# Kernel optimization log

Hardware: AMD Instinct MI355X
Metric: run time of the kernel (lower is better)

Reference implementation:

```python
import jax, jax.numpy as jnp
import numpy as np
import math

B, S, D, H, DK, DFF = 64, 512, 512, 8, 64, 2048


def _layernorm(x, g, b, eps=1e-5):
    mu = jnp.mean(x, axis=-1, keepdims=True)
    var = jnp.var(x, axis=-1, keepdims=True)
    return (x - mu) * jax.lax.rsqrt(var + eps) * g + b


def setup_inputs() -> dict:
    key = jax.random.key(0)
    ks = jax.random.split(key, 16)
    std = 0.02
    return {
        "query": jax.random.normal(ks[0], (B, S, D), jnp.float32),
        "key": jax.random.normal(ks[1], (B, S, D), jnp.float32),
        "values": jax.random.normal(ks[2], (B, S, D), jnp.float32),
        "forget_rate": jax.random.uniform(ks[3], (B, 1, S, 1), jnp.float32),
        "Wq": jax.random.normal(ks[4], (D, D), jnp.float32) * std,
        "bq": jnp.zeros((D,), jnp.float32),
        "Wk": jax.random.normal(ks[5], (D, D), jnp.float32) * std,
        "bk": jnp.zeros((D,), jnp.float32),
        "Wv": jax.random.normal(ks[6], (D, D), jnp.float32) * std,
        "bv": jnp.zeros((D,), jnp.float32),
        "Wo": jax.random.normal(ks[7], (D, D), jnp.float32) * std,
        "bo": jnp.zeros((D,), jnp.float32),
        "g1": jnp.ones((D,), jnp.float32),
        "beta1": jnp.zeros((D,), jnp.float32),
        "W1": jax.random.normal(ks[8], (D, DFF), jnp.float32) * std,
        "bf1": jnp.zeros((DFF,), jnp.float32),
        "W2": jax.random.normal(ks[9], (DFF, D), jnp.float32) * std,
        "bf2": jnp.zeros((D,), jnp.float32),
        "g2": jnp.ones((D,), jnp.float32),
        "beta2": jnp.zeros((D,), jnp.float32),
        "mask": 0,
    }


def reference(query, key, values, forget_rate, Wq, bq, Wk, bk, Wv, bv, Wo, bo,
              g1, beta1, W1, bf1, W2, bf2, g2, beta2, mask):
    bs, seqlen, _ = query.shape
    # project and split heads -> [B, H, S, DK]
    q = (query @ Wq + bq).reshape(bs, seqlen, H, DK).transpose(0, 2, 1, 3)
    k = (key @ Wk + bk).reshape(bs, seqlen, H, DK).transpose(0, 2, 1, 3)
    v = (values @ Wv + bv).reshape(bs, seqlen, H, DK).transpose(0, 2, 1, 3)

    scores = jnp.einsum('bhqd,bhkd->bhqk', q, k) / math.sqrt(DK)  # [B,H,S,S]
    # forget_rate [B,1,S,1] broadcasts over heads and key dim (== repeat in torch)
    scores = scores * forget_rate
    # src_mask: allowed where triu(ones, k=mask) == 0, i.e. j < i + mask
    allowed = jnp.tril(jnp.ones((seqlen, seqlen), bool), mask - 1)
    scores = jnp.where(allowed, scores, jnp.float32(-1e32))
    probs = jax.nn.softmax(scores, axis=-1)
    if mask == 0:  # zero_pad: overwrite first query row with zeros
        probs = probs.at[:, :, 0, :].set(0.0)
    out = jnp.einsum('bhqk,bhkd->bhqd', probs, v)  # [B,H,S,DK]
    concat = out.transpose(0, 2, 1, 3).reshape(bs, seqlen, D)
    attn_out = concat @ Wo + bo

    x = _layernorm(query + attn_out, g1, beta1)
    ff = jax.nn.relu(x @ W1 + bf1) @ W2 + bf2
    x = _layernorm(x + ff, g2, beta2)
    return x
```

## Files before the change

### kernel.cpp

```cpp
#include <hip/hip_runtime.h>
#include <hip/hip_bf16.h>
#include <stdint.h>

typedef __attribute__((ext_vector_type(8))) short short8;
typedef __attribute__((ext_vector_type(8))) unsigned short ushort8;
typedef __attribute__((ext_vector_type(4))) unsigned short ushort4v;
typedef __attribute__((ext_vector_type(4))) float f32x4;

#define DEV static __device__ __forceinline__

constexpr int Bc = 64, Sc = 512, Dc = 512, Hc = 8, DKc = 64, DFc = 2048;
constexpr int Mtot = Bc * Sc;
constexpr int CB   = 16;
constexpr int RC   = CB * Sc;

DEV unsigned short f2b(float f) {
    union { float f; unsigned u; } x; x.f = f;
    unsigned r = x.u + 0x7fffu + ((x.u >> 16) & 1u);
    return (unsigned short)(r >> 16);
}
DEV float b2f(unsigned short u) {
    union { unsigned u; float f; } x; x.u = ((unsigned)u) << 16; return x.f;
}

DEV void gload16(const void* g, void* l) {
    __builtin_amdgcn_global_load_lds(
        (const __attribute__((address_space(1))) void*)g,
        (__attribute__((address_space(3))) void*)l, 16, 0, 0);
}

__global__ void k_cvt(const float* __restrict__ in, unsigned short* __restrict__ out, int n8) {
    int idx = blockIdx.x * 256 + threadIdx.x;
    if (idx >= n8) return;
    const float4* p = (const float4*)(in + (size_t)idx * 8);
    float4 a = p[0], b = p[1];
    ushort8 o;
    o[0] = f2b(a.x); o[1] = f2b(a.y); o[2] = f2b(a.z); o[3] = f2b(a.w);
    o[4] = f2b(b.x); o[5] = f2b(b.y); o[6] = f2b(b.z); o[7] = f2b(b.w);
    *(ushort8*)(out + (size_t)idx * 8) = o;
}

__global__ void k_copy8(const unsigned short* __restrict__ in, unsigned short* __restrict__ out, int n8) {
    int idx = blockIdx.x * 256 + threadIdx.x;
    if (idx >= n8) return;
    *(ushort8*)(out + (size_t)idx * 8) = *(const ushort8*)(in + (size_t)idx * 8);
}

__global__ void k_cvt_w_all(
    const float* __restrict__ Wq, const float* __restrict__ Wk, const float* __restrict__ Wv,
    const float* __restrict__ Wo, const float* __restrict__ W1, const float* __restrict__ W2,
    unsigned short* __restrict__ Wqt, unsigned short* __restrict__ Wkt,
    unsigned short* __restrict__ Wvt, unsigned short* __restrict__ Wot,
    unsigned short* __restrict__ W1t, unsigned short* __restrict__ W2t) {
    int idx = blockIdx.x * 256 + threadIdx.x;
    const float* in; unsigned short* out; int K, N, li;
    if (idx < 131072) {
        int w = idx >> 15, r = idx & 32767;
        const float* ins[4] = {Wq, Wk, Wv, Wo};
        unsigned short* outs[4] = {Wqt, Wkt, Wvt, Wot};
        in = ins[w]; out = outs[w]; K = 512; N = 512; li = r;
    } else if (idx < 262144) {
        in = W1; out = W1t; K = 512; N = 2048; li = idx - 131072;
    } else {
        in = W2; out = W2t; K = 2048; N = 512; li = idx - 262144;
    }
    int kc = li % (K / 8), n = li / (K / 8);
    ushort8 o;
    #pragma unroll
    for (int j = 0; j < 8; ++j) o[j] = f2b(in[(size_t)(kc * 8 + j) * N + n]);
    *(ushort8*)(out + (size_t)n * K + kc * 8) = o;
}

__global__ void k_cvt_all(
    const float* __restrict__ Wq, const float* __restrict__ Wk, const float* __restrict__ Wv,
    const float* __restrict__ Wo, const float* __restrict__ W1, const float* __restrict__ W2,
    unsigned short* __restrict__ Wqt, unsigned short* __restrict__ Wkt,
    unsigned short* __restrict__ Wvt, unsigned short* __restrict__ Wot,
    unsigned short* __restrict__ W1t, unsigned short* __restrict__ W2t,
    const float* __restrict__ q_in, const float* __restrict__ k_in, const float* __restrict__ v_in,
    unsigned short* __restrict__ q_out, unsigned short* __restrict__ k_out,
    unsigned short* __restrict__ v_out) {
    int idx = blockIdx.x * 256 + threadIdx.x;
    if (idx >= 393216) {
        int a = idx - 393216;
        const float* in; unsigned short* out; int li;
        if (a < 2097152)       { in = q_in; out = q_out; li = a; }
        else if (a < 4194304)  { in = k_in; out = k_out; li = a - 2097152; }
        else                   { in = v_in; out = v_out; li = a - 4194304; }
        const float4* p = (const float4*)(in + (size_t)li * 8);
        float4 x = p[0], y = p[1];
        ushort8 o;
        o[0] = f2b(x.x); o[1] = f2b(x.y); o[2] = f2b(x.z); o[3] = f2b(x.w);
        o[4] = f2b(y.x); o[5] = f2b(y.y); o[6] = f2b(y.z); o[7] = f2b(y.w);
        *(ushort8*)(out + (size_t)li * 8) = o;
        return;
    }
    const float* in; unsigned short* out; int K, N, li;
    if (idx < 131072) {
        int w = idx >> 15, r = idx & 32767;
        const float* ins[4] = {Wq, Wk, Wv, Wo};
        unsigned short* outs[4] = {Wqt, Wkt, Wvt, Wot};
        in = ins[w]; out = outs[w]; K = 512; N = 512; li = r;
    } else if (idx < 262144) {
        in = W1; out = W1t; K = 512; N = 2048; li = idx - 131072;
    } else {
        in = W2; out = W2t; K = 2048; N = 512; li = idx - 262144;
    }
    int kc = li % (K / 8), n = li / (K / 8);
    ushort8 o;
    #pragma unroll
    for (int j = 0; j < 8; ++j) o[j] = f2b(in[(size_t)(kc * 8 + j) * N + n]);
    *(ushort8*)(out + (size_t)n * K + kc * 8) = o;
}

template<int BM, int BN>
DEV void gemm_core(const unsigned short* __restrict__ A, int lda,
                   const unsigned short* __restrict__ Bt, int ldb, int K,
                   unsigned short* lA, unsigned short* lB,
                   f32x4 (&acc)[BM / 32][BN / 32]) {
    constexpr int MF = BM / 32, NF = BN / 32;
    const int tid = threadIdx.x, lane = tid & 63, wv = tid >> 6;
    const int wr = wv >> 1, wc = wv & 1;
    const int l15 = lane & 15, l4 = lane >> 4, l7 = l15 & 7;
    #pragma unroll
    for (int mf = 0; mf < MF; ++mf)
        #pragma unroll
        for (int nf = 0; nf < NF; ++nf)
            acc[mf][nf] = f32x4{0.f, 0.f, 0.f, 0.f};

    auto stage = [&](int buf, int kt0) {
        unsigned short* dA = lA + (size_t)buf * BM * 64;
        #pragma unroll
        for (int r = 0; r < BM / 32; ++r) {
            int c = r * 256 + tid, row = c >> 3, gs = c & 7;
            gload16(A + (size_t)row * lda + kt0 + ((gs ^ (row & 7)) * 8),
                    dA + (size_t)(r * 256 + wv * 64) * 8);
        }
        unsigned short* dB = lB + (size_t)buf * BN * 64;
        #pragma unroll
        for (int r = 0; r < BN / 32; ++r) {
            int c = r * 256 + tid, row = c >> 3, gs = c & 7;
            gload16(Bt + (size_t)row * ldb + kt0 + ((gs ^ (row & 7)) * 8),
                    dB + (size_t)(r * 256 + wv * 64) * 8);
        }
    };

    stage(0, 0);
    __syncthreads();
    const int nk = K / 64;
    for (int t = 0; t < nk; ++t) {
        const int buf = t & 1;
        if (t + 1 < nk) stage(buf ^ 1, (t + 1) * 64);
        const unsigned short* cA = lA + (size_t)buf * BM * 64;
        const unsigned short* cB = lB + (size_t)buf * BN * 64;
        #pragma unroll
        for (int kt = 0; kt < 2; ++kt) {
            short8 af[MF], bfr[NF];
            #pragma unroll
            for (int mf = 0; mf < MF; ++mf)
                af[mf] = *(const short8*)&cA[(wr * (BM / 2) + mf * 16 + l15) * 64 +
                                             (((kt * 4 + l4) ^ l7) * 8)];
            #pragma unroll
            for (int nf = 0; nf < NF; ++nf)
                bfr[nf] = *(const short8*)&cB[(wc * (BN / 2) + nf * 16 + l15) * 64 +
                                              (((kt * 4 + l4) ^ l7) * 8)];
            #pragma unroll
            for (int mf = 0; mf < MF; ++mf)
                #pragma unroll
                for (int nf = 0; nf < NF; ++nf)
                    acc[mf][nf] = __builtin_amdgcn_mfma_f32_16x16x32_bf16(af[mf], bfr[nf], acc[mf][nf], 0, 0, 0);
        }
        __syncthreads();
    }
}

__global__ __launch_bounds__(256) void k_gemm_qkv(
    const unsigned short* __restrict__ X, const unsigned short* __restrict__ Wt,
    const float* __restrict__ bias, unsigned short* __restrict__ out, int which) {
    __shared__ unsigned short lA[2 * 128 * 64], lB[2 * 128 * 64];
    int m0 = blockIdx.x * 128, n0 = blockIdx.y * 128;
    f32x4 acc[4][4];
    gemm_core<128, 128>(X + (size_t)m0 * Dc, Dc, Wt + (size_t)n0 * Dc, Dc, Dc, lA, lB, acc);
    const int lane = threadIdx.x & 63, wv = threadIdx.x >> 6;
    const int wr = wv >> 1, wc = wv & 1, l15 = lane & 15, l4 = lane >> 4;
    #pragma unroll
    for (int mf = 0; mf < 4; ++mf) {
        #pragma unroll
        for (int nf = 0; nf < 4; ++nf) {
            int n = n0 + wc * 64 + nf * 16 + l15;
            int h = n >> 6, dk = n & 63;
            float bv = bias[n];
            if (which == 2) {
                int mg = m0 + wr * 64 + mf * 16 + l4 * 4;
                int b = mg >> 9, s = mg & 511;
                ushort4v o;
                #pragma unroll
                for (int r = 0; r < 4; ++r) o[r] = f2b(acc[mf][nf][r] + bv);
                *(ushort4v*)&out[((size_t)(b * Hc + h) * DKc + dk) * Sc + s] = o;
            } else {
                float scale = (which == 0) ? 0.125f : 1.0f;
                #pragma unroll
                for (int r = 0; r < 4; ++r) {
                    int mg = m0 + wr * 64 + mf * 16 + l4 * 4 + r;
                    int b = mg >> 9, s = mg & 511;
                    out[((size_t)(b * Hc + h) * Sc + s) * DKc + dk] = f2b((acc[mf][nf][r] + bv) * scale);
                }
            }
        }
    }
}

__global__ __launch_bounds__(256) void k_flash(
    const unsigned short* __restrict__ Qb, const unsigned short* __restrict__ Kb,
    const unsigned short* __restrict__ Vt, unsigned short* __restrict__ conc,
    const float* __restrict__ fr, const int* __restrict__ maskp, int b_base) {
    __shared__ unsigned short lKb[2][64 * 64];
    __shared__ unsigned short lVb[2][64 * 64];
    __shared__ unsigned short lP[128 * 64];
    const int head = blockIdx.y, bl = head >> 3, h = head & 7;
    const int bg = b_base + bl;
    const int m0 = blockIdx.x * 128;
    const int mv = *maskp;
    const int tid = threadIdx.x, lane = tid & 63, w = tid >> 6;
    const int l15 = lane & 15, l4 = lane >> 4;
    const int l7 = l15 & 7;
    const int rw = w * 32;
    constexpr float LOG2E = 1.44269504088896340736f;

    unsigned short* lQ = &lKb[0][0];
    const unsigned short* Qg = Qb + ((size_t)head * Sc + m0) * DKc;
    #pragma unroll
    for (int r = 0; r < 4; ++r) {
        int c = r * 256 + tid, row = c >> 3, gs = c & 7;
        gload16(Qg + (size_t)row * DKc + ((gs ^ (row & 7)) * 8), lQ + (size_t)(r * 256 + w * 64) * 8);
    }
    __syncthreads();
    short8 qf[2][2];
    #pragma unroll
    for (int kt = 0; kt < 2; ++kt)
        #pragma unroll
        for (int mf = 0; mf < 2; ++mf)
            qf[kt][mf] = *(const short8*)&lQ[(rw + mf * 16 + l15) * 64 + (((kt * 4 + l4) ^ l7) * 8)];
    float frr[8];
    #pragma unroll
    for (int mf = 0; mf < 2; ++mf)
        #pragma unroll
        for (int r = 0; r < 4; ++r)
            frr[mf * 4 + r] = fr[(size_t)bg * Sc + m0 + rw + mf * 16 + l4 * 4 + r] * LOG2E;
    __syncthreads();

    f32x4 accO[2][4];
    #pragma unroll
    for (int mf = 0; mf < 2; ++mf)
        #pragma unroll
        for (int nf = 0; nf < 4; ++nf)
            accO[mf][nf] = f32x4{0.f, 0.f, 0.f, 0.f};
    float l_run[8];
    #pragma unroll
    for (int i = 0; i < 8; ++i) l_run[i] = 0.f;

    const unsigned short* Kg0 = Kb + (size_t)head * Sc * DKc;
    const unsigned short* Vg0 = Vt + (size_t)head * DKc * Sc;
    int nt = ((m0 + 126 + mv) >> 7) + 1;
    if (nt > 4) nt = 4;
    if (nt < 1) nt = 1;
    const int nc = nt * 2;

    {
        const unsigned short* Kg = Kg0;
        const unsigned short* Vg = Vg0;
        #pragma unroll
        for (int r = 0; r < 2; ++r) {
            int c = r * 256 + tid, row = c >> 3, gs = c & 7;
            gload16(Kg + (size_t)row * DKc + ((gs ^ (row & 7)) * 8), &lKb[0][0] + (size_t)(r * 256 + w * 64) * 8);
            gload16(Vg + (size_t)row * Sc + ((gs ^ (row & 7)) * 8), &lVb[0][0] + (size_t)(r * 256 + w * 64) * 8);
        }
    }
    __syncthreads();

    for (int ci = 0; ci < nc; ++ci) {
        const int buf = ci & 1;
        if (ci + 1 < nc) {
            int n1 = (ci + 1) * 64;
            const unsigned short* Kg = Kg0 + (size_t)n1 * DKc;
            const unsigned short* Vg = Vg0 + n1;
            #pragma unroll
            for (int r = 0; r < 2; ++r) {
                int c = r * 256 + tid, row = c >> 3, gs = c & 7;
                gload16(Kg + (size_t)row * DKc + ((gs ^ (row & 7)) * 8),
                        &lKb[buf ^ 1][0] + (size_t)(r * 256 + w * 64) * 8);
                gload16(Vg + (size_t)row * Sc + ((gs ^ (row & 7)) * 8),
                        &lVb[buf ^ 1][0] + (size_t)(r * 256 + w * 64) * 8);
            }
        }
        const int n0c = ci * 64;
        short8 bk[4][2];
        #pragma unroll
        for (int j = 0; j < 4; ++j)
            #pragma unroll
            for (int kt = 0; kt < 2; ++kt)
                bk[j][kt] = *(const short8*)&lKb[buf][(j * 16 + l15) * 64 + (((kt * 4 + l4) ^ l7) * 8)];
        #pragma unroll
        for (int mf = 0; mf < 2; ++mf) {
            f32x4 sa[4];
            #pragma unroll
            for (int j = 0; j < 4; ++j) sa[j] = f32x4{0.f, 0.f, 0.f, 0.f};
            #pragma unroll
            for (int kt = 0; kt < 2; ++kt)
                #pragma unroll
                for (int j = 0; j < 4; ++j)
                    sa[j] = __builtin_amdgcn_mfma_f32_16x16x32_bf16(qf[kt][mf], bk[j][kt], sa[j], 0, 0, 0);
            #pragma unroll
            for (int r = 0; r < 4; ++r) {
                int rowl = rw + mf * 16 + l4 * 4 + r;
                int rowg = m0 + rowl;
                int prs = rowl & 7;
                float fres = frr[mf * 4 + r];
                float ps = 0.f;
                #pragma unroll
                for (int j = 0; j < 4; ++j) {
                    int colg = n0c + j * 16 + l15;
                    float p = (colg < rowg + mv) ? exp2f(sa[j][r] * fres) : 0.f;
                    ps += p;
                    int gw = j * 2 + (l15 >> 3);
                    lP[rowl * 64 + ((gw ^ prs) * 8) + l7] = f2b(p);
                }
                l_run[mf * 4 + r] += ps;
            }
        }
        #pragma unroll
        for (int kl = 0; kl < 2; ++kl) {
            short8 pa[2];
            #pragma unroll
            for (int mf = 0; mf < 2; ++mf)
                pa[mf] = *(const short8*)&lP[(rw + mf * 16 + l15) * 64 + (((kl * 4 + l4) ^ l7) * 8)];
            #pragma unroll
            for (int nf = 0; nf < 4; ++nf) {
                short8 bv8 = *(const short8*)&lVb[buf][(nf * 16 + l15) * 64 + (((kl * 4 + l4) ^ l7) * 8)];
                #pragma unroll
                for (int mf = 0; mf < 2; ++mf)
                    accO[mf][nf] = __builtin_amdgcn_mfma_f32_16x16x32_bf16(pa[mf], bv8, accO[mf][nf], 0, 0, 0);
            }
        }
        __syncthreads();
    }
    #pragma unroll
    for (int mf = 0; mf < 2; ++mf)
        #pragma unroll
        for (int r = 0; r < 4; ++r) {
            int rowg = m0 + rw + mf * 16 + l4 * 4 + r;
            float l = l_run[mf * 4 + r];
            #pragma unroll
            for (int o = 1; o < 16; o <<= 1) l += __shfl_xor(l, o);
            float inv = (rowg + mv > 0) ? 1.0f / l : 0.f;
            #pragma unroll
            for (int nf = 0; nf < 4; ++nf) {
                int dk = nf * 16 + l15;
                conc[((size_t)bg * Sc + rowg) * Dc + h * DKc + dk] = f2b(accO[mf][nf][r] * inv);
            }
        }
}

__global__ __launch_bounds__(256) void k_wo(
    const unsigned short* __restrict__ Cc, const unsigned short* __restrict__ Wot,
    const float* __restrict__ bo, const float* __restrict__ query, float* __restrict__ y) {
    __shared__ unsigned short lA[2 * 128 * 64], lB[2 * 128 * 64];
    int m0 = blockIdx.x * 128, n0 = blockIdx.y * 128;
    f32x4 acc[4][4];
    gemm_core<128, 128>(Cc + (size_t)m0 * Dc, Dc, Wot + (size_t)n0 * Dc, Dc, Dc, lA, lB, acc);
    const int lane = threadIdx.x & 63, wv = threadIdx.x >> 6;
    const int wr = wv >> 1, wc = wv & 1, l15 = lane & 15, l4 = lane >> 4;
    #pragma unroll
    for (int mf = 0; mf < 4; ++mf)
        #pragma unroll
        for (int nf = 0; nf < 4; ++nf) {
            int n = n0 + wc * 64 + nf * 16 + l15;
            float bv = bo[n];
            #pragma unroll
            for (int r = 0; r < 4; ++r) {
                int m = m0 + wr * 64 + mf * 16 + l4 * 4 + r;
                y[(size_t)m * Dc + n] = acc[mf][nf][r] + bv + query[(size_t)m * Dc + n];
            }
        }
}

__global__ __launch_bounds__(256) void k_ff1(
    const unsigned short* __restrict__ X, const unsigned short* __restrict__ W1t,
    const float* __restrict__ b1, unsigned short* __restrict__ hb) {
    __shared__ unsigned short lA[2 * 128 * 64], lB[2 * 128 * 64];
    int m0 = blockIdx.x * 128, n0 = blockIdx.y * 128;
    f32x4 acc[4][4];
    gemm_core<128, 128>(X + (size_t)m0 * Dc, Dc, W1t + (size_t)n0 * Dc, Dc, Dc, lA, lB, acc);
    const int lane = threadIdx.x & 63, wv = threadIdx.x >> 6;
    const int wr = wv >> 1, wc = wv & 1, l15 = lane & 15, l4 = lane >> 4;
    #pragma unroll
    for (int mf = 0; mf < 4; ++mf)
        #pragma unroll
        for (int nf = 0; nf < 4; ++nf) {
            int n = n0 + wc * 64 + nf * 16 + l15;
            float bv = b1[n];
            #pragma unroll
            for (int r = 0; r < 4; ++r) {
                int m = m0 + wr * 64 + mf * 16 + l4 * 4 + r;
                hb[(size_t)m * DFc + n] = f2b(fmaxf(acc[mf][nf][r] + bv, 0.f));
            }
        }
}

__global__ __launch_bounds__(256) void k_ff2b(
    const unsigned short* __restrict__ Hb, const unsigned short* __restrict__ W2t,
    const float* __restrict__ b2, const unsigned short* __restrict__ residb,
    float* __restrict__ y) {
    __shared__ unsigned short lA[2 * 128 * 64], lB[2 * 128 * 64];
    int m0 = blockIdx.x * 128, n0 = blockIdx.y * 128;
    f32x4 acc[4][4];
    gemm_core<128, 128>(Hb + (size_t)m0 * DFc, DFc, W2t + (size_t)n0 * DFc, DFc, DFc, lA, lB, acc);
    const int lane = threadIdx.x & 63, wv = threadIdx.x >> 6;
    const int wr = wv >> 1, wc = wv & 1, l15 = lane & 15, l4 = lane >> 4;
    #pragma unroll
    for (int mf = 0; mf < 4; ++mf)
        #pragma unroll
        for (int nf = 0; nf < 4; ++nf) {
            int n = n0 + wc * 64 + nf * 16 + l15;
            float bv = b2[n];
            #pragma unroll
            for (int r = 0; r < 4; ++r) {
                int m = m0 + wr * 64 + mf * 16 + l4 * 4 + r;
                y[(size_t)m * Dc + n] = acc[mf][nf][r] + bv + b2f(residb[(size_t)m * Dc + n]);
            }
        }
}

__global__ __launch_bounds__(256) void k_ln(
    const float* __restrict__ in, const float* __restrict__ g, const float* __restrict__ be,
    float* __restrict__ outf, unsigned short* __restrict__ outb) {
    int rid = blockIdx.x * 4 + (threadIdx.x >> 6);
    int lane = threadIdx.x & 63;
    const float* row = in + (size_t)rid * Dc;
    float4 a = ((const float4*)row)[lane * 2];
    float4 b = ((const float4*)row)[lane * 2 + 1];
    float x[8] = {a.x, a.y, a.z, a.w, b.x, b.y, b.z, b.w};
    float s = 0.f, ss = 0.f;
    #pragma unroll
    for (int j = 0; j < 8; ++j) { s += x[j]; ss += x[j] * x[j]; }
    #pragma unroll
    for (int o = 1; o < 64; o <<= 1) { s += __shfl_xor(s, o); ss += __shfl_xor(ss, o); }
    float mu = s * (1.f / 512.f);
    float var = ss * (1.f / 512.f) - mu * mu;
    float rs = rsqrtf(var + 1e-5f);
    float4 g0 = ((const float4*)g)[lane * 2], g1v = ((const float4*)g)[lane * 2 + 1];
    float4 e0 = ((const float4*)be)[lane * 2], e1 = ((const float4*)be)[lane * 2 + 1];
    float gg[8] = {g0.x, g0.y, g0.z, g0.w, g1v.x, g1v.y, g1v.z, g1v.w};
    float ee[8] = {e0.x, e0.y, e0.z, e0.w, e1.x, e1.y, e1.z, e1.w};
    float o8[8];
    #pragma unroll
    for (int j = 0; j < 8; ++j) o8[j] = (x[j] - mu) * rs * gg[j] + ee[j];
    if (outf) {
        float4* po = (float4*)(outf + (size_t)rid * Dc);
        float4 w0 = {o8[0], o8[1], o8[2], o8[3]}, w1 = {o8[4], o8[5], o8[6], o8[7]};
        po[lane * 2] = w0; po[lane * 2 + 1] = w1;
    }
    if (outb) {
        ushort8 ob;
        #pragma unroll
        for (int j = 0; j < 8; ++j) ob[j] = f2b(o8[j]);
        *(ushort8*)(outb + (size_t)rid * Dc + lane * 8) = ob;
    }
}

extern "C" void kernel_launch(void* const* d_in, const int* in_sizes, int n_in,
                              void* d_out, int out_size, void* d_ws, size_t ws_size,
                              hipStream_t stream) {
    const float* query = (const float*)d_in[0];
    const float* key_  = (const float*)d_in[1];
    const float* vals  = (const float*)d_in[2];
    const float* fr    = (const float*)d_in[3];
    const float* Wq = (const float*)d_in[4];  const float* bq = (const float*)d_in[5];
    const float* Wk = (const float*)d_in[6];  const float* bk = (const float*)d_in[7];
    const float* Wv = (const float*)d_in[8];  const float* bv = (const float*)d_in[9];
    const float* Wo = (const float*)d_in[10]; const float* bo = (const float*)d_in[11];
    const float* g1 = (const float*)d_in[12]; const float* be1 = (const float*)d_in[13];
    const float* W1 = (const float*)d_in[14]; const float* b1 = (const float*)d_in[15];
    const float* W2 = (const float*)d_in[16]; const float* b2 = (const float*)d_in[17];
    const float* g2 = (const float*)d_in[18]; const float* be2 = (const float*)d_in[19];
    const int* maskp = (const int*)d_in[20];
    float* out = (float*)d_out;

    char* ab = (char*)d_out;
    unsigned short* xb    = (unsigned short*)ab;
    unsigned short* conc  = (unsigned short*)ab;
    unsigned short* x1b   = conc;
    unsigned short* keyst = (unsigned short*)(ab + (size_t)32 * 1048576);
    unsigned short* Qc   = (unsigned short*)(ab + (size_t)32 * 1048576);
    unsigned short* Kc   = (unsigned short*)(ab + (size_t)40 * 1048576);
    unsigned short* Vc   = (unsigned short*)(ab + (size_t)48 * 1048576);
    unsigned short* xst  = (unsigned short*)(ab + (size_t)56 * 1048576);
    float*          xfc  = (float*)(ab + (size_t)32 * 1048576);

    char* ws = (char*)d_ws;
    unsigned short* Wqt = (unsigned short*)ws;
    unsigned short* Wkt = Wqt + 512 * 512;
    unsigned short* Wvt = Wkt + 512 * 512;
    unsigned short* Wot = Wvt + 512 * 512;
    unsigned short* W1t = Wot + 512 * 512;
    unsigned short* W2t = W1t + 2048 * 512;
    char* wend = (char*)(W2t + 512 * 2048);
    size_t wrem = (ws_size > (size_t)(wend - ws)) ? ws_size - (size_t)(wend - ws) : 0;
    const size_t qkvb = (size_t)Mtot * Dc * 2;

    const bool bigpath = (wrem >= 3 * qkvb);

    const float* acts[3] = {query, key_, vals};
    const unsigned short* wt3[3] = {Wqt, Wkt, Wvt};
    const float* bs3[3] = {bq, bk, bv};

    if (bigpath) {
        unsigned short* QbF = (unsigned short*)wend;
        unsigned short* KbF = QbF + qkvb / 2;
        unsigned short* VtF = KbF + qkvb / 2;
        unsigned short* hb     = QbF;
        unsigned short* resid0 = VtF;
        float*          xf     = (float*)KbF;
        const int Mc = 16384;

        k_cvt_all<<<dim3(26112), dim3(256), 0, stream>>>(
            Wq, Wk, Wv, Wo, W1, W2, Wqt, Wkt, Wvt, Wot, W1t, W2t,
            query, key_, vals, xb, keyst, KbF);

        k_gemm_qkv<<<dim3(Mtot / 128, 4), dim3(256), 0, stream>>>(KbF,   Wvt, bv, VtF, 2);
        k_gemm_qkv<<<dim3(Mtot / 128, 4), dim3(256), 0, stream>>>(keyst, Wkt, bk, KbF, 1);
        k_gemm_qkv<<<dim3(Mtot / 128, 4), dim3(256), 0, stream>>>(xb,    Wqt, bq, QbF, 0);

        k_flash<<<dim3(Sc / 128, Bc * Hc), dim3(256), 0, stream>>>(QbF, KbF, VtF, conc, fr, maskp, 0);

        k_wo<<<dim3(Mtot / 128, 4), dim3(256), 0, stream>>>(conc, Wot, bo, query, xf);
        k_ln<<<dim3(Mtot / 4), dim3(256), 0, stream>>>(xf, g1, be1, (float*)nullptr, x1b);

        k_copy8<<<dim3(Mc / 4), dim3(256), 0, stream>>>(x1b, resid0, Mc * Dc / 8);

        for (int mb = Mtot - Mc; mb >= 0; mb -= Mc) {
            k_ff1<<<dim3(Mc / 128, 16), dim3(256), 0, stream>>>(x1b + (size_t)mb * Dc, W1t, b1, hb);
            k_ff2b<<<dim3(Mc / 128, 4), dim3(256), 0, stream>>>(hb, W2t, b2,
                                                                mb ? x1b + (size_t)mb * Dc : resid0,
                                                                out + (size_t)mb * Dc);
            k_ln<<<dim3(Mc / 4), dim3(256), 0, stream>>>(out + (size_t)mb * Dc, g2, be2,
                                                         out + (size_t)mb * Dc, (unsigned short*)nullptr);
        }
    } else {
        int Mc = 128;
        for (int c = 8192; c >= 128; c >>= 1)
            if ((size_t)c * 5120 <= wrem) { Mc = c; break; }
        unsigned short* hb     = (unsigned short*)wend;
        unsigned short* resid0 = (unsigned short*)(wend + (size_t)Mc * 4096);

        k_cvt_w_all<<<dim3(1536), dim3(256), 0, stream>>>(Wq, Wk, Wv, Wo, W1, W2,
                                                          Wqt, Wkt, Wvt, Wot, W1t, W2t);
        unsigned short* out3[3] = {Qc, Kc, Vc};
        for (int cb = 0; cb < Bc / CB; ++cb) {
            for (int p = 0; p < 3; ++p) {
                k_cvt<<<dim3(RC * Dc / 8 / 256), dim3(256), 0, stream>>>(
                    acts[p] + (size_t)cb * RC * Dc, xst, RC * Dc / 8);
                k_gemm_qkv<<<dim3(RC / 128, 4), dim3(256), 0, stream>>>(xst, wt3[p], bs3[p], out3[p], p);
            }
            k_flash<<<dim3(Sc / 128, CB * Hc), dim3(256), 0, stream>>>(Qc, Kc, Vc, conc, fr, maskp, cb * CB);
        }
        for (int hp = 0; hp < 2; ++hp) {
            int mb = hp * 16384;
            k_wo<<<dim3(16384 / 128, 4), dim3(256), 0, stream>>>(conc + (size_t)mb * Dc, Wot, bo,
                                                                 query + (size_t)mb * Dc, xfc);
            k_ln<<<dim3(16384 / 4), dim3(256), 0, stream>>>(xfc, g1, be1, (float*)nullptr,
                                                            x1b + (size_t)mb * Dc);
        }
        k_copy8<<<dim3(Mc / 4), dim3(256), 0, stream>>>(x1b, resid0, Mc * Dc / 8);
        for (int mb = Mtot - Mc; mb >= 0; mb -= Mc) {
            k_ff1<<<dim3(Mc / 128, 16), dim3(256), 0, stream>>>(x1b + (size_t)mb * Dc, W1t, b1, hb);
            k_ff2b<<<dim3(Mc / 128, 4), dim3(256), 0, stream>>>(hb, W2t, b2,
                                                                mb ? x1b + (size_t)mb * Dc : resid0,
                                                                out + (size_t)mb * Dc);
            k_ln<<<dim3(Mc / 4), dim3(256), 0, stream>>>(out + (size_t)mb * Dc, g2, be2,
                                                         out + (size_t)mb * Dc, (unsigned short*)nullptr);
        }
    }
}
```

Baseline: 576.3 us.

## Triple-buffer GEMM K-tiles with BK=32 and manual waitcnt barriers

Rewrites the shared GEMM mainloop to use three LDS stages of 32-wide K tiles instead of two stages of 64-wide tiles. Two tiles are prefetched ahead, and per-iteration synchronisation is replaced with explicit vmcnt/lgkmcnt waits and a single raw s_barrier. The XOR swizzle is changed to match the 4-chunk row layout. The aim is to keep more global loads in flight and drop one barrier per step while cutting LDS per block. The cost is twice as many loop iterations with less MFMA work between barriers, and correctness depends on the hard-coded vmcnt literal matching the load count.

```diff
diff --git a/kernel.cpp b/kernel.cpp
--- a/kernel.cpp
+++ b/kernel.cpp
@@ -118,10 +118,11 @@
                    const unsigned short* __restrict__ Bt, int ldb, int K,
                    unsigned short* lA, unsigned short* lB,
                    f32x4 (&acc)[BM / 32][BN / 32]) {
+    static_assert(BM == 128 && BN == 128, "vmcnt(4) literal assumes 4 gloads/thread/stage");
     constexpr int MF = BM / 32, NF = BN / 32;
     const int tid = threadIdx.x, lane = tid & 63, wv = tid >> 6;
     const int wr = wv >> 1, wc = wv & 1;
-    const int l15 = lane & 15, l4 = lane >> 4, l7 = l15 & 7;
+    const int l15 = lane & 15, l4 = lane >> 4;
     #pragma unroll
     for (int mf = 0; mf < MF; ++mf)
         #pragma unroll
@@ -129,55 +130,59 @@
             acc[mf][nf] = f32x4{0.f, 0.f, 0.f, 0.f};
 
     auto stage = [&](int buf, int kt0) {
-        unsigned short* dA = lA + (size_t)buf * BM * 64;
-        #pragma unroll
-        for (int r = 0; r < BM / 32; ++r) {
-            int c = r * 256 + tid, row = c >> 3, gs = c & 7;
-            gload16(A + (size_t)row * lda + kt0 + ((gs ^ (row & 7)) * 8),
+        unsigned short* dA = lA + (size_t)buf * BM * 32;
+        #pragma unroll
+        for (int r = 0; r < BM / 64; ++r) {
+            int c = r * 256 + tid, row = c >> 2, gs = c & 3;
+            int key = (row ^ (row >> 2)) & 3;
+            gload16(A + (size_t)row * lda + kt0 + ((gs ^ key) * 8),
                     dA + (size_t)(r * 256 + wv * 64) * 8);
         }
-        unsigned short* dB = lB + (size_t)buf * BN * 64;
-        #pragma unroll
-        for (int r = 0; r < BN / 32; ++r) {
-            int c = r * 256 + tid, row = c >> 3, gs = c & 7;
-            gload16(Bt + (size_t)row * ldb + kt0 + ((gs ^ (row & 7)) * 8),
+        unsigned short* dB = lB + (size_t)buf * BN * 32;
+        #pragma unroll
+        for (int r = 0; r < BN / 64; ++r) {
+            int c = r * 256 + tid, row = c >> 2, gs = c & 3;
+            int key = (row ^ (row >> 2)) & 3;
+            gload16(Bt + (size_t)row * ldb + kt0 + ((gs ^ key) * 8),
                     dB + (size_t)(r * 256 + wv * 64) * 8);
         }
     };
 
+    const int nk = K / 32;
     stage(0, 0);
-    __syncthreads();
-    const int nk = K / 64;
+    stage(1, 32);
     for (int t = 0; t < nk; ++t) {
-        const int buf = t & 1;
-        if (t + 1 < nk) stage(buf ^ 1, (t + 1) * 64);
-        const unsigned short* cA = lA + (size_t)buf * BM * 64;
-        const unsigned short* cB = lB + (size_t)buf * BN * 64;
-        #pragma unroll
-        for (int kt = 0; kt < 2; ++kt) {
-            short8 af[MF], bfr[NF];
-            #pragma unroll
-            for (int mf = 0; mf < MF; ++mf)
-                af[mf] = *(const short8*)&cA[(wr * (BM / 2) + mf * 16 + l15) * 64 +
-                                             (((kt * 4 + l4) ^ l7) * 8)];
+        asm volatile("s_waitcnt lgkmcnt(0)" ::: "memory");
+        if (t + 1 < nk) asm volatile("s_waitcnt vmcnt(4)" ::: "memory");
+        else            asm volatile("s_waitcnt vmcnt(0)" ::: "memory");
+        asm volatile("s_barrier" ::: "memory");
+        __builtin_amdgcn_sched_barrier(0);
+        if (t + 2 < nk) stage((t + 2) % 3, (t + 2) * 32);
+        const unsigned short* cA = lA + (size_t)(t % 3) * BM * 32;
+        const unsigned short* cB = lB + (size_t)(t % 3) * BN * 32;
+        short8 af[MF], bfr[NF];
+        #pragma unroll
+        for (int mf = 0; mf < MF; ++mf) {
+            int row = wr * (BM / 2) + mf * 16 + l15;
+            af[mf] = *(const short8*)&cA[(size_t)row * 32 + ((l4 ^ ((row ^ (row >> 2)) & 3)) * 8)];
+        }
+        #pragma unroll
+        for (int nf = 0; nf < NF; ++nf) {
+            int row = wc * (BN / 2) + nf * 16 + l15;
+            bfr[nf] = *(const short8*)&cB[(size_t)row * 32 + ((l4 ^ ((row ^ (row >> 2)) & 3)) * 8)];
+        }
+        #pragma unroll
+        for (int mf = 0; mf < MF; ++mf)
             #pragma unroll
             for (int nf = 0; nf < NF; ++nf)
-                bfr[nf] = *(const short8*)&cB[(wc * (BN / 2) + nf * 16 + l15) * 64 +
-                                              (((kt * 4 + l4) ^ l7) * 8)];
-            #pragma unroll
-            for (int mf = 0; mf < MF; ++mf)
-                #pragma unroll
-                for (int nf = 0; nf < NF; ++nf)
-                    acc[mf][nf] = __builtin_amdgcn_mfma_f32_16x16x32_bf16(af[mf], bfr[nf], acc[mf][nf], 0, 0, 0);
-        }
-        __syncthreads();
+                acc[mf][nf] = __builtin_amdgcn_mfma_f32_16x16x32_bf16(af[mf], bfr[nf], acc[mf][nf], 0, 0, 0);
     }
 }
 
 __global__ __launch_bounds__(256) void k_gemm_qkv(
     const unsigned short* __restrict__ X, const unsigned short* __restrict__ Wt,
     const float* __restrict__ bias, unsigned short* __restrict__ out, int which) {
-    __shared__ unsigned short lA[2 * 128 * 64], lB[2 * 128 * 64];
+    __shared__ unsigned short lA[3 * 128 * 32], lB[3 * 128 * 32];
     int m0 = blockIdx.x * 128, n0 = blockIdx.y * 128;
     f32x4 acc[4][4];
     gemm_core<128, 128>(X + (size_t)m0 * Dc, Dc, Wt + (size_t)n0 * Dc, Dc, Dc, lA, lB, acc);
@@ -364,7 +369,7 @@
 __global__ __launch_bounds__(256) void k_wo(
     const unsigned short* __restrict__ Cc, const unsigned short* __restrict__ Wot,
     const float* __restrict__ bo, const float* __restrict__ query, float* __restrict__ y) {
-    __shared__ unsigned short lA[2 * 128 * 64], lB[2 * 128 * 64];
+    __shared__ unsigned short lA[3 * 128 * 32], lB[3 * 128 * 32];
     int m0 = blockIdx.x * 128, n0 = blockIdx.y * 128;
     f32x4 acc[4][4];
     gemm_core<128, 128>(Cc + (size_t)m0 * Dc, Dc, Wot + (size_t)n0 * Dc, Dc, Dc, lA, lB, acc);
@@ -387,7 +392,7 @@
 __global__ __launch_bounds__(256) void k_ff1(
     const unsigned short* __restrict__ X, const unsigned short* __restrict__ W1t,
     const float* __restrict__ b1, unsigned short* __restrict__ hb) {
-    __shared__ unsigned short lA[2 * 128 * 64], lB[2 * 128 * 64];
+    __shared__ unsigned short lA[3 * 128 * 32], lB[3 * 128 * 32];
     int m0 = blockIdx.x * 128, n0 = blockIdx.y * 128;
     f32x4 acc[4][4];
     gemm_core<128, 128>(X + (size_t)m0 * Dc, Dc, W1t + (size_t)n0 * Dc, Dc, Dc, lA, lB, acc);
@@ -411,7 +416,7 @@
     const unsigned short* __restrict__ Hb, const unsigned short* __restrict__ W2t,
     const float* __restrict__ b2, const unsigned short* __restrict__ residb,
     float* __restrict__ y) {
-    __shared__ unsigned short lA[2 * 128 * 64], lB[2 * 128 * 64];
+    __shared__ unsigned short lA[3 * 128 * 32], lB[3 * 128 * 32];
     int m0 = blockIdx.x * 128, n0 = blockIdx.y * 128;
     f32x4 acc[4][4];
     gemm_core<128, 128>(Hb + (size_t)m0 * DFc, DFc, W2t + (size_t)n0 * DFc, DFc, DFc, lA, lB, acc);
```

Measured after the change: 581.5 us. Within noise of the previous version (+0.9%).
